# Kernel optimization log

Hardware: AMD Instinct MI355X
Metric: run time of the kernel (lower is better)

The kernel has to match this reference:

```python
import jax, jax.numpy as jnp
import numpy as np

B = 262144
C = 195  # number of countries
EARTH_R = 6371.0  # km


def setup_inputs() -> dict:
    key = jax.random.key(0)
    k1, k2, k3, k4 = jax.random.split(key, 4)
    logits = jax.random.normal(k1, (B, C), dtype=jnp.float32)
    target = jax.random.randint(k2, (B,), 0, C)
    # country coordinates: lat in [-90, 90], lon in [-180, 180]
    lat = jax.random.uniform(k3, (C,), minval=-90.0, maxval=90.0, dtype=jnp.float32)
    lon = jax.random.uniform(k4, (C,), minval=-180.0, maxval=180.0, dtype=jnp.float32)
    coords = jnp.stack([lat, lon], axis=-1)  # [C, 2]
    return {"logits": logits, "target": target, "coords": coords}


def _haversine(lat1, lon1, lat2, lon2):
    lat1, lon1, lat2, lon2 = map(jnp.deg2rad, (lat1, lon1, lat2, lon2))
    dlat = lat2 - lat1
    dlon = lon2 - lon1
    a = jnp.sin(dlat / 2) ** 2 + jnp.cos(lat1) * jnp.cos(lat2) * jnp.sin(dlon / 2) ** 2
    return 2.0 * EARTH_R * jnp.arcsin(jnp.sqrt(a))


def reference(logits, target, coords):
    # cross entropy (mean reduction)
    logp = jax.nn.log_softmax(logits, axis=-1)  # [B, C]
    ce_loss = -jnp.take_along_axis(logp, target[:, None], axis=1).mean()
    # geographical loss: haversine between argmax-pred country and true country
    preds = jnp.argmax(logits, axis=1)  # [B]
    pc = coords[preds]   # [B, 2]
    tc = coords[target]  # [B, 2]
    dist = _haversine(pc[:, 0], pc[:, 1], tc[:, 0], tc[:, 1])  # [B]
    geo_loss = dist.mean() / 500.0
    return ce_loss + geo_loss
```

## Files before the change

kernel.cpp:

```cpp
#include <hip/hip_runtime.h>
#include <hip/hip_bf16.h>
#include <math.h>

#define NC 195
#define ROWS_PER_CHUNK 16
#define CHUNKS_PER_BLOCK 4
#define BLOCK_ROWS (ROWS_PER_CHUNK * CHUNKS_PER_BLOCK)
#define F4_PER_CHUNK (ROWS_PER_CHUNK * NC / 4)

template<int CTRL>
__device__ __forceinline__ float dpp_f(float v) {
    int i = __float_as_int(v);
    return __int_as_float(__builtin_amdgcn_update_dpp(i, i, CTRL, 0xF, 0xF, false));
}
template<int CTRL>
__device__ __forceinline__ int dpp_i(int v) {
    return __builtin_amdgcn_update_dpp(v, v, CTRL, 0xF, 0xF, false);
}

__device__ __forceinline__ float hav_scaled(float lat1, float lon1, float lat2, float lon2) {
    const float d2r = 0.017453292519943295f;
    lat1 *= d2r; lon1 *= d2r; lat2 *= d2r; lon2 *= d2r;
    float sdlat = sinf(0.5f * (lat2 - lat1));
    float sdlon = sinf(0.5f * (lon2 - lon1));
    float a = sdlat * sdlat + cosf(lat1) * cosf(lat2) * sdlon * sdlon;
    a = fminf(fmaxf(a, 0.0f), 1.0f);
    return (2.0f * 6371.0f / 500.0f) * asinf(sqrtf(a));
}

__global__ __launch_bounds__(256) void main_kernel(const float4* __restrict__ logits4,
                                                   const int* __restrict__ target,
                                                   const float* __restrict__ coords,
                                                   float* __restrict__ partials) {
    __shared__ float lds[ROWS_PER_CHUNK * NC];
    __shared__ int tgt[BLOCK_ROWS];
    __shared__ float wpart[16];
    const int t = threadIdx.x;
    float4* lds4 = (float4*)lds;

    const long long row0 = (long long)blockIdx.x * BLOCK_ROWS;
    if (t < BLOCK_ROWS) tgt[t] = target[row0 + t];

    const long long base4 = (long long)blockIdx.x * CHUNKS_PER_BLOCK * F4_PER_CHUNK;

    float4 n0 = logits4[base4 + t];
    float4 n1 = logits4[base4 + t + 256];
    float4 n2 = logits4[base4 + t + 512];
    float4 n3;
    if (t < F4_PER_CHUNK - 768) n3 = logits4[base4 + t + 768];
    lds4[t] = n0; lds4[t + 256] = n1; lds4[t + 512] = n2;
    if (t < F4_PER_CHUNK - 768) lds4[t + 768] = n3;
    __syncthreads();

    const int u = t & 15;
    const int r = t >> 4;
    const float* __restrict__ rowp = lds + r * NC;
    float acc = 0.0f;

    for (int i = 0; i < CHUNKS_PER_BLOCK; ++i) {
        const bool has_next = (i + 1 < CHUNKS_PER_BLOCK);
        if (has_next) {
            const long long nb = base4 + (long long)(i + 1) * F4_PER_CHUNK;
            n0 = logits4[nb + t];
            n1 = logits4[nb + t + 256];
            n2 = logits4[nb + t + 512];
            if (t < F4_PER_CHUNK - 768) n3 = logits4[nb + t + 768];
        }

        float x[13];
        #pragma unroll
        for (int k = 0; k < 12; ++k) x[k] = rowp[u + 16 * k];
        x[12] = (u < 3) ? rowp[192 + u] : -INFINITY;

        float m = x[0]; int mi = u;
        #pragma unroll
        for (int k = 1; k < 13; ++k) {
            if (x[k] > m) { m = x[k]; mi = u + 16 * k; }
        }
        {
            float om; int oi;
            om = dpp_f<0xB1>(m);  oi = dpp_i<0xB1>(mi);
            if (om > m || (om == m && oi < mi)) { m = om; mi = oi; }
            om = dpp_f<0x4E>(m);  oi = dpp_i<0x4E>(mi);
            if (om > m || (om == m && oi < mi)) { m = om; mi = oi; }
            om = dpp_f<0x141>(m); oi = dpp_i<0x141>(mi);
            if (om > m || (om == m && oi < mi)) { m = om; mi = oi; }
            om = dpp_f<0x140>(m); oi = dpp_i<0x140>(mi);
            if (om > m || (om == m && oi < mi)) { m = om; mi = oi; }
        }
        float s = 0.0f;
        #pragma unroll
        for (int k = 0; k < 13; ++k) s += __expf(x[k] - m);
        s += dpp_f<0xB1>(s);
        s += dpp_f<0x4E>(s);
        s += dpp_f<0x141>(s);
        s += dpp_f<0x140>(s);

        if (u == 0) {
            int tg = tgt[i * ROWS_PER_CHUNK + r];
            float ce = (m + __logf(s)) - rowp[tg];
            acc += ce + hav_scaled(coords[2 * mi], coords[2 * mi + 1],
                                   coords[2 * tg], coords[2 * tg + 1]);
        }
        __syncthreads();
        if (has_next) {
            lds4[t] = n0; lds4[t + 256] = n1; lds4[t + 512] = n2;
            if (t < F4_PER_CHUNK - 768) lds4[t + 768] = n3;
            __syncthreads();
        }
    }

    if (u == 0) wpart[r] = acc;
    __syncthreads();
    if (t == 0) {
        float v = 0.0f;
        #pragma unroll
        for (int j = 0; j < 16; ++j) v += wpart[j];
        partials[blockIdx.x] = v;
    }
}

__global__ __launch_bounds__(1024) void reduce_kernel(const float* __restrict__ partials,
                                                      float inv_b, float* __restrict__ out) {
    float s = partials[threadIdx.x] + partials[threadIdx.x + 1024]
            + partials[threadIdx.x + 2048] + partials[threadIdx.x + 3072];
    #pragma unroll
    for (int off = 32; off > 0; off >>= 1) s += __shfl_xor(s, off);
    __shared__ float ws[16];
    if ((threadIdx.x & 63) == 0) ws[threadIdx.x >> 6] = s;
    __syncthreads();
    if (threadIdx.x == 0) {
        float tot = 0.0f;
        #pragma unroll
        for (int w = 0; w < 16; ++w) tot += ws[w];
        out[0] = tot * inv_b;
    }
}

extern "C" void kernel_launch(void* const* d_in, const int* in_sizes, int n_in,
                              void* d_out, int out_size, void* d_ws, size_t ws_size,
                              hipStream_t stream) {
    const float* logits = (const float*)d_in[0];
    const int*   target = (const int*)d_in[1];
    const float* coords = (const float*)d_in[2];
    float* out = (float*)d_out;

    const int B = in_sizes[1];
    const int n_blocks = B / BLOCK_ROWS;

    float* partials = (float*)d_ws;

    main_kernel<<<n_blocks, 256, 0, stream>>>((const float4*)logits, target, coords, partials);
    reduce_kernel<<<1, 1024, 0, stream>>>(partials, 1.0f / (float)B, out);
}
```

Measured before the change: 43.79 us.

## Make each wave stage its own rows in private LDS, removing block barriers

The block-wide chunk staging, where all 256 threads load 16 rows into shared LDS and sync, becomes per-wave staging. Each wave owns 16 rows, stages 4 rows at a time into its own LDS slice and loops without __syncthreads. Targets are read directly from global memory instead of being staged in LDS. This removes block-level barriers and cross-wave stalls. It relies on wave-level lockstep for LDS write/read ordering, and with no explicit wave barrier or fence that ordering is fragile.

```diff
diff --git a/kernel.cpp b/kernel.cpp
--- a/kernel.cpp
+++ b/kernel.cpp
@@ -3,10 +3,10 @@
 #include <math.h>
 
 #define NC 195
-#define ROWS_PER_CHUNK 16
-#define CHUNKS_PER_BLOCK 4
-#define BLOCK_ROWS (ROWS_PER_CHUNK * CHUNKS_PER_BLOCK)
-#define F4_PER_CHUNK (ROWS_PER_CHUNK * NC / 4)
+#define WCHUNKS 4
+#define WAVE_ROWS 16
+#define BLOCK_ROWS 64
+#define F4_PER_WCHUNK 195
 
 template<int CTRL>
 __device__ __forceinline__ float dpp_f(float v) {
@@ -32,39 +32,38 @@
                                                    const int* __restrict__ target,
                                                    const float* __restrict__ coords,
                                                    float* __restrict__ partials) {
-    __shared__ float lds[ROWS_PER_CHUNK * NC];
-    __shared__ int tgt[BLOCK_ROWS];
+    __shared__ float lds[4 * 780];
     __shared__ float wpart[16];
     const int t = threadIdx.x;
-    float4* lds4 = (float4*)lds;
+    const int wave = t >> 6;
+    const int lane = t & 63;
+    const int u = lane & 15;
+    const int g = lane >> 4;
+    float* __restrict__ wlds = lds + wave * 780;
+    float4* wlds4 = (float4*)wlds;
 
-    const long long row0 = (long long)blockIdx.x * BLOCK_ROWS;
-    if (t < BLOCK_ROWS) tgt[t] = target[row0 + t];
+    const long long rows0 = (long long)blockIdx.x * BLOCK_ROWS + wave * WAVE_ROWS;
+    const long long gq = (rows0 >> 2) * NC;
 
-    const long long base4 = (long long)blockIdx.x * CHUNKS_PER_BLOCK * F4_PER_CHUNK;
+    float4 n0 = logits4[gq + lane];
+    float4 n1 = logits4[gq + lane + 64];
+    float4 n2 = logits4[gq + lane + 128];
+    float4 n3;
+    if (lane < 3) n3 = logits4[gq + lane + 192];
+    wlds4[lane] = n0; wlds4[lane + 64] = n1; wlds4[lane + 128] = n2;
+    if (lane < 3) wlds4[lane + 192] = n3;
 
-    float4 n0 = logits4[base4 + t];
-    float4 n1 = logits4[base4 + t + 256];
-    float4 n2 = logits4[base4 + t + 512];
-    float4 n3;
-    if (t < F4_PER_CHUNK - 768) n3 = logits4[base4 + t + 768];
-    lds4[t] = n0; lds4[t + 256] = n1; lds4[t + 512] = n2;
-    if (t < F4_PER_CHUNK - 768) lds4[t + 768] = n3;
-    __syncthreads();
-
-    const int u = t & 15;
-    const int r = t >> 4;
-    const float* __restrict__ rowp = lds + r * NC;
+    const float* __restrict__ rowp = wlds + g * NC;
     float acc = 0.0f;
 
-    for (int i = 0; i < CHUNKS_PER_BLOCK; ++i) {
-        const bool has_next = (i + 1 < CHUNKS_PER_BLOCK);
+    for (int c = 0; c < WCHUNKS; ++c) {
+        const bool has_next = (c + 1 < WCHUNKS);
         if (has_next) {
-            const long long nb = base4 + (long long)(i + 1) * F4_PER_CHUNK;
-            n0 = logits4[nb + t];
-            n1 = logits4[nb + t + 256];
-            n2 = logits4[nb + t + 512];
-            if (t < F4_PER_CHUNK - 768) n3 = logits4[nb + t + 768];
+            const long long nb = gq + (long long)(c + 1) * F4_PER_WCHUNK;
+            n0 = logits4[nb + lane];
+            n1 = logits4[nb + lane + 64];
+            n2 = logits4[nb + lane + 128];
+            if (lane < 3) n3 = logits4[nb + lane + 192];
         }
 
         float x[13];
@@ -97,20 +96,20 @@
         s += dpp_f<0x140>(s);
 
         if (u == 0) {
-            int tg = tgt[i * ROWS_PER_CHUNK + r];
+            const long long row = rows0 + c * 4 + g;
+            int tg = target[row];
             float ce = (m + __logf(s)) - rowp[tg];
             acc += ce + hav_scaled(coords[2 * mi], coords[2 * mi + 1],
                                    coords[2 * tg], coords[2 * tg + 1]);
         }
-        __syncthreads();
+
         if (has_next) {
-            lds4[t] = n0; lds4[t + 256] = n1; lds4[t + 512] = n2;
-            if (t < F4_PER_CHUNK - 768) lds4[t + 768] = n3;
-            __syncthreads();
+            wlds4[lane] = n0; wlds4[lane + 64] = n1; wlds4[lane + 128] = n2;
+            if (lane < 3) wlds4[lane + 192] = n3;
         }
     }
 
-    if (u == 0) wpart[r] = acc;
+    if (u == 0) wpart[wave * 4 + g] = acc;
     __syncthreads();
     if (t == 0) {
         float v = 0.0f;
```

After: 45.59 us. 4.1% more time.

## Double-buffer LDS chunks and use 32 lanes per row with 8-row chunks

Applied to the files above, without the earlier changes.

Switches the staging buffer to two LDS buffers so the next chunk is written while the current one is still being read, removing one __syncthreads per chunk. Chunks shrink to 8 rows processed by 32 lanes each, which cuts per-thread register prefetch to two float4 loads and needs an extra cross-row shuffle in each reduction. The cost is more loop iterations and barriers per block, and only two loads in flight per thread to hide memory latency.

```diff
diff --git a/kernel.cpp b/kernel.cpp
--- a/kernel.cpp
+++ b/kernel.cpp
@@ -3,10 +3,10 @@
 #include <math.h>
 
 #define NC 195
-#define ROWS_PER_CHUNK 16
-#define CHUNKS_PER_BLOCK 4
-#define BLOCK_ROWS (ROWS_PER_CHUNK * CHUNKS_PER_BLOCK)
-#define F4_PER_CHUNK (ROWS_PER_CHUNK * NC / 4)
+#define ROWS_PER_CHUNK 8
+#define CHUNKS 8
+#define BLOCK_ROWS 64
+#define F4_PER_CHUNK 390
 
 template<int CTRL>
 __device__ __forceinline__ float dpp_f(float v) {
@@ -32,50 +32,47 @@
                                                    const int* __restrict__ target,
                                                    const float* __restrict__ coords,
                                                    float* __restrict__ partials) {
-    __shared__ float lds[ROWS_PER_CHUNK * NC];
+    __shared__ float buf[2][ROWS_PER_CHUNK * NC];
     __shared__ int tgt[BLOCK_ROWS];
-    __shared__ float wpart[16];
+    __shared__ float wpart[8];
     const int t = threadIdx.x;
-    float4* lds4 = (float4*)lds;
-
     const long long row0 = (long long)blockIdx.x * BLOCK_ROWS;
     if (t < BLOCK_ROWS) tgt[t] = target[row0 + t];
 
-    const long long base4 = (long long)blockIdx.x * CHUNKS_PER_BLOCK * F4_PER_CHUNK;
+    const long long base4 = (row0 >> 2) * NC;
 
-    float4 n0 = logits4[base4 + t];
-    float4 n1 = logits4[base4 + t + 256];
-    float4 n2 = logits4[base4 + t + 512];
-    float4 n3;
-    if (t < F4_PER_CHUNK - 768) n3 = logits4[base4 + t + 768];
-    lds4[t] = n0; lds4[t + 256] = n1; lds4[t + 512] = n2;
-    if (t < F4_PER_CHUNK - 768) lds4[t + 768] = n3;
+    float4 a0 = logits4[base4 + t];
+    float4 a1;
+    if (t < F4_PER_CHUNK - 256) a1 = logits4[base4 + 256 + t];
+    {
+        float4* d = (float4*)buf[0];
+        d[t] = a0;
+        if (t < F4_PER_CHUNK - 256) d[256 + t] = a1;
+    }
     __syncthreads();
 
-    const int u = t & 15;
-    const int r = t >> 4;
-    const float* __restrict__ rowp = lds + r * NC;
+    const int u = t & 31;
+    const int g = t >> 5;
     float acc = 0.0f;
 
-    for (int i = 0; i < CHUNKS_PER_BLOCK; ++i) {
-        const bool has_next = (i + 1 < CHUNKS_PER_BLOCK);
+    for (int c = 0; c < CHUNKS; ++c) {
+        const bool has_next = (c + 1 < CHUNKS);
         if (has_next) {
-            const long long nb = base4 + (long long)(i + 1) * F4_PER_CHUNK;
-            n0 = logits4[nb + t];
-            n1 = logits4[nb + t + 256];
-            n2 = logits4[nb + t + 512];
-            if (t < F4_PER_CHUNK - 768) n3 = logits4[nb + t + 768];
+            const long long nb = base4 + (long long)(c + 1) * F4_PER_CHUNK;
+            a0 = logits4[nb + t];
+            if (t < F4_PER_CHUNK - 256) a1 = logits4[nb + 256 + t];
         }
 
-        float x[13];
+        const float* __restrict__ rowp = buf[c & 1] + g * NC;
+        float x[7];
         #pragma unroll
-        for (int k = 0; k < 12; ++k) x[k] = rowp[u + 16 * k];
-        x[12] = (u < 3) ? rowp[192 + u] : -INFINITY;
+        for (int k = 0; k < 6; ++k) x[k] = rowp[u + 32 * k];
+        x[6] = (u < 3) ? rowp[192 + u] : -INFINITY;
 
         float m = x[0]; int mi = u;
         #pragma unroll
-        for (int k = 1; k < 13; ++k) {
-            if (x[k] > m) { m = x[k]; mi = u + 16 * k; }
+        for (int k = 1; k < 7; ++k) {
+            if (x[k] > m) { m = x[k]; mi = u + 32 * k; }
         }
         {
             float om; int oi;
@@ -87,35 +84,39 @@
             if (om > m || (om == m && oi < mi)) { m = om; mi = oi; }
             om = dpp_f<0x140>(m); oi = dpp_i<0x140>(mi);
             if (om > m || (om == m && oi < mi)) { m = om; mi = oi; }
+            om = __shfl_xor(m, 16); oi = __shfl_xor(mi, 16);
+            if (om > m || (om == m && oi < mi)) { m = om; mi = oi; }
         }
         float s = 0.0f;
         #pragma unroll
-        for (int k = 0; k < 13; ++k) s += __expf(x[k] - m);
+        for (int k = 0; k < 7; ++k) s += __expf(x[k] - m);
         s += dpp_f<0xB1>(s);
         s += dpp_f<0x4E>(s);
         s += dpp_f<0x141>(s);
         s += dpp_f<0x140>(s);
+        s += __shfl_xor(s, 16);
 
         if (u == 0) {
-            int tg = tgt[i * ROWS_PER_CHUNK + r];
+            int tg = tgt[c * ROWS_PER_CHUNK + g];
             float ce = (m + __logf(s)) - rowp[tg];
             acc += ce + hav_scaled(coords[2 * mi], coords[2 * mi + 1],
                                    coords[2 * tg], coords[2 * tg + 1]);
         }
+
+        if (has_next) {
+            float4* d = (float4*)buf[(c + 1) & 1];
+            d[t] = a0;
+            if (t < F4_PER_CHUNK - 256) d[256 + t] = a1;
+        }
         __syncthreads();
-        if (has_next) {
-            lds4[t] = n0; lds4[t + 256] = n1; lds4[t + 512] = n2;
-            if (t < F4_PER_CHUNK - 768) lds4[t + 768] = n3;
-            __syncthreads();
-        }
     }
 
-    if (u == 0) wpart[r] = acc;
+    if (u == 0) wpart[g] = acc;
     __syncthreads();
     if (t == 0) {
         float v = 0.0f;
         #pragma unroll
-        for (int j = 0; j < 16; ++j) v += wpart[j];
+        for (int j = 0; j < 8; ++j) v += wpart[j];
         partials[blockIdx.x] = v;
     }
 }
```

New measurement: 60.14 us. +37.3%, slower.
